# Optimization experiments

Hardware: AMD Instinct MI355X
Metric: run time of the kernel (lower is better)

Reference implementation:

```python
import jax, jax.numpy as jnp
import numpy as np

N = 131072   # total gates/nodes in the batched block-diagonal circuit graph
E = 524288   # directed edges (avg degree 4)
D = 100      # hidden dim
DA = 50      # msg MLP hidden
DC = 30      # classifier hidden
R = 20       # message-passing rounds


def mlp(x, W1, b1, W2, b2):
    return jax.nn.relu(x @ W1 + b1) @ W2 + b2


def gru_step(x, h, Wih, Whh, bih, bhh):
    # single-timestep torch.nn.GRU cell
    gi = x @ Wih.T + bih
    gh = h @ Whh.T + bhh
    ir, iz, inn = jnp.split(gi, 3, axis=-1)
    hr, hz, hn = jnp.split(gh, 3, axis=-1)
    r = jax.nn.sigmoid(ir + hr)
    z = jax.nn.sigmoid(iz + hz)
    nwe = jnp.tanh(inn + r * hn)
    return (1.0 - z) * nwe + z * h


def setup_inputs():
    key = jax.random.key(0)
    ks = jax.random.split(key, 26)
    s = 0.05

    def rn(k, shape):
        return jax.random.normal(k, shape, dtype=jnp.float32) * s

    inp = {
        'features': jax.random.normal(ks[0], (N, 4), dtype=jnp.float32),
        'edge_row': jax.random.randint(ks[1], (E,), 0, N, dtype=jnp.int32),
        'edge_col': jax.random.randint(ks[2], (E,), 0, N, dtype=jnp.int32),
        'init_W': rn(ks[3], (4, D)), 'init_b': jnp.zeros((D,), jnp.float32),
        'fmsg_W1': rn(ks[4], (D, DA)), 'fmsg_b1': jnp.zeros((DA,), jnp.float32),
        'fmsg_W2': rn(ks[5], (DA, D)), 'fmsg_b2': jnp.zeros((D,), jnp.float32),
        'bmsg_W1': rn(ks[6], (D, DA)), 'bmsg_b1': jnp.zeros((DA,), jnp.float32),
        'bmsg_W2': rn(ks[7], (DA, D)), 'bmsg_b2': jnp.zeros((D,), jnp.float32),
        'fgru_Wih': rn(ks[8], (3 * D, D)), 'fgru_Whh': rn(ks[9], (3 * D, D)),
        'fgru_bih': jnp.zeros((3 * D,), jnp.float32), 'fgru_bhh': jnp.zeros((3 * D,), jnp.float32),
        'bgru_Wih': rn(ks[10], (3 * D, D)), 'bgru_Whh': rn(ks[11], (3 * D, D)),
        'bgru_bih': jnp.zeros((3 * D,), jnp.float32), 'bgru_bhh': jnp.zeros((3 * D,), jnp.float32),
        'cls_W1': rn(ks[12], (D, DC)), 'cls_b1': jnp.zeros((DC,), jnp.float32),
        'cls_W2': rn(ks[13], (DC, 1)), 'cls_b2': jnp.zeros((1,), jnp.float32),
    }
    return inp


def reference(features, edge_row, edge_col, init_W, init_b,
              fmsg_W1, fmsg_b1, fmsg_W2, fmsg_b2,
              bmsg_W1, bmsg_b1, bmsg_W2, bmsg_b2,
              fgru_Wih, fgru_Whh, fgru_bih, fgru_bhh,
              bgru_Wih, bgru_Whh, bgru_bih, bgru_bhh,
              cls_W1, cls_b1, cls_W2, cls_b2):
    n = features.shape[0]
    h = features @ init_W + init_b  # [N, D]

    def round_body(h, _):
        # forward pass: adj @ forward_msg(h)
        fm = mlp(h, fmsg_W1, fmsg_b1, fmsg_W2, fmsg_b2)
        f_msg = jax.ops.segment_sum(fm[edge_col], edge_row, num_segments=n)
        h = gru_step(f_msg, h, fgru_Wih, fgru_Whh, fgru_bih, fgru_bhh)
        # backward pass: adj.T @ backward_msg(h)
        bm = mlp(h, bmsg_W1, bmsg_b1, bmsg_W2, bmsg_b2)
        b_msg = jax.ops.segment_sum(bm[edge_row], edge_col, num_segments=n)
        h = gru_step(b_msg, h, bgru_Wih, bgru_Whh, bgru_bih, bgru_bhh)
        return h, None

    h, _ = jax.lax.scan(jax.checkpoint(round_body), h, None, length=R)
    return mlp(h, cls_W1, cls_b1, cls_W2, cls_b2)  # [N, 1]
```

## Files before the change

### kernel.cpp

```cpp
#include <hip/hip_runtime.h>
#include <math.h>

#define Nn 131072
#define Ee 524288

typedef __attribute__((ext_vector_type(8))) short short8;
typedef __attribute__((ext_vector_type(4))) float f32x4;
typedef unsigned short ushort_t;
typedef unsigned int uint32;

__device__ __forceinline__ f32x4 mfma16(short8 a, short8 b, f32x4 c) {
    return __builtin_amdgcn_mfma_f32_16x16x32_bf16(a, b, c, 0, 0, 0);
}

__device__ __forceinline__ uint32 rne_bf16(float x) {
    uint32 u = __float_as_uint(x);
    return (u + 0x7FFFu + ((u >> 16) & 1u)) >> 16;
}

__device__ __forceinline__ void split3(float x, uint32& h, uint32& m, uint32& l) {
    h = rne_bf16(x);
    float hf = __uint_as_float(h << 16);
    float r1 = x - hf;
    m = rne_bf16(r1);
    float mf = __uint_as_float(m << 16);
    float r2 = r1 - mf;
    l = rne_bf16(r2);
}

__global__ void diag_kernel(float* out, float val) {
    int n = blockIdx.x * 256 + threadIdx.x;
    if (n < Nn) out[n] = (n == 0) ? val : 0.f;
}
__global__ void zero_ints(int* p, int n) {
    int i = blockIdx.x * 256 + threadIdx.x;
    if (i < n) p[i] = 0;
}

__global__ void hist_kernel(const int* __restrict__ er, const int* __restrict__ ec,
                            int* __restrict__ cnt_f, int* __restrict__ cnt_b) {
    int e = blockIdx.x * 256 + threadIdx.x;
    atomicAdd(&cnt_f[er[e]], 1);
    atomicAdd(&cnt_b[ec[e]], 1);
}

__global__ __launch_bounds__(1024) void scan_kernel(const int* __restrict__ cnt,
                                                    int* __restrict__ ptr, int n) {
    __shared__ int sums[1024];
    int t = threadIdx.x;
    int chunk = n >> 10;
    int base = t * chunk;
    int s = 0;
    for (int i = 0; i < chunk; i++) s += cnt[base + i];
    sums[t] = s;
    __syncthreads();
    for (int off = 1; off < 1024; off <<= 1) {
        int v = (t >= off) ? sums[t - off] : 0;
        __syncthreads();
        sums[t] += v;
        __syncthreads();
    }
    int run = (t == 0) ? 0 : sums[t - 1];
    for (int i = 0; i < chunk; i++) { ptr[base + i] = run; run += cnt[base + i]; }
    if (t == 1023) ptr[n] = run;
}

__global__ void fill_kernel(const int* __restrict__ er, const int* __restrict__ ec,
                            int* __restrict__ ptr_f, int* __restrict__ ptr_b,
                            int* __restrict__ src_f, int* __restrict__ src_b) {
    int e = blockIdx.x * 256 + threadIdx.x;
    int r = er[e], c = ec[e];
    int p = atomicAdd(&ptr_f[r], 1); src_f[p] = c;
    int q = atomicAdd(&ptr_b[c], 1); src_b[q] = r;
}

__global__ void prep_gru_w(const float* __restrict__ Wih, const float* __restrict__ Whh,
                           const float* __restrict__ bih, const float* __restrict__ bhh,
                           ushort_t* __restrict__ W0, ushort_t* __restrict__ W1,
                           ushort_t* __restrict__ W2, float* __restrict__ bg) {
    int gid = blockIdx.x * 256 + threadIdx.x;
    if (gid >= 448 * 224) return;
    int c = gid / 224, k = gid - c * 224;
    int d = c >> 2, g = c & 3;
    float w = 0.f;
    if (d < 100) {
        if (k < 100) {
            if (g == 0)      w = Wih[d * 100 + k];
            else if (g == 1) w = Wih[(100 + d) * 100 + k];
            else if (g == 2) w = Wih[(200 + d) * 100 + k];
        } else if (k < 200) {
            int kk = k - 100;
            if (g == 0)      w = Whh[d * 100 + kk];
            else if (g == 1) w = Whh[(100 + d) * 100 + kk];
            else if (g == 3) w = Whh[(200 + d) * 100 + kk];
        }
    }
    uint32 h, m, l; split3(w, h, m, l);
    W0[gid] = (ushort_t)h; W1[gid] = (ushort_t)m; W2[gid] = (ushort_t)l;
    if (k == 0) {
        float b = 0.f;
        if (d < 100) {
            if (g == 0)      b = bih[d] + bhh[d];
            else if (g == 1) b = bih[100 + d] + bhh[100 + d];
            else if (g == 2) b = bih[200 + d];
            else             b = bhh[200 + d];
        }
        bg[c] = b;
    }
}

__global__ void prep_msg_w(const float* __restrict__ W1, const float* __restrict__ b1,
                           const float* __restrict__ W2, const float* __restrict__ b2,
                           ushort_t* __restrict__ A0, ushort_t* __restrict__ A1,
                           ushort_t* __restrict__ A2, float* __restrict__ b1p,
                           ushort_t* __restrict__ B0, ushort_t* __restrict__ B1,
                           ushort_t* __restrict__ B2, float* __restrict__ b2p) {
    int gid = blockIdx.x * 256 + threadIdx.x;
    if (gid < 8192) {
        int c = gid >> 7, k = gid & 127;
        float w = (c < 50 && k < 100) ? W1[k * 50 + c] : 0.f;
        uint32 h, m, l; split3(w, h, m, l);
        A0[gid] = (ushort_t)h; A1[gid] = (ushort_t)m; A2[gid] = (ushort_t)l;
        if (k == 0) b1p[c] = (c < 50) ? b1[c] : 0.f;
    } else if (gid < 8192 + 7168) {
        int t = gid - 8192;
        int c = t >> 6, k = t & 63;
        float w = (c < 100 && k < 50) ? W2[k * 100 + c] : 0.f;
        uint32 h, m, l; split3(w, h, m, l);
        B0[t] = (ushort_t)h; B1[t] = (ushort_t)m; B2[t] = (ushort_t)l;
        if (k == 0) b2p[c] = (c < 100) ? b2[c] : 0.f;
    }
}

__global__ void init_h_kernel(const float* __restrict__ feat, const float* __restrict__ W,
                              const float* __restrict__ b, float* __restrict__ Act) {
    int gid = blockIdx.x * 256 + threadIdx.x;
    int n = gid / 100, d = gid - n * 100;
    float acc = b[d];
#pragma unroll
    for (int k = 0; k < 4; k++) acc += feat[n * 4 + k] * W[k * 100 + d];
    Act[(size_t)n * 200 + 100 + d] = acc;
}

__global__ __launch_bounds__(256, 2) void msg_mfma(
    const float* __restrict__ Act,
    const ushort_t* __restrict__ A0, const ushort_t* __restrict__ A1,
    const ushort_t* __restrict__ A2, const float* __restrict__ b1p,
    const ushort_t* __restrict__ B0, const ushort_t* __restrict__ B1,
    const ushort_t* __restrict__ B2, const float* __restrict__ b2p,
    float* __restrict__ fm) {
    __shared__ ushort_t C1[3][64][72];
    const int tid = threadIdx.x;
    const int u = tid >> 6;
    const int lane = tid & 63;
    const int m = lane & 15, q = lane >> 4;
    const int n0 = blockIdx.x * 64;
    const int n = n0 + u * 16 + m;

    f32x4 z = {0.f, 0.f, 0.f, 0.f};
    f32x4 a1[4] = {z, z, z, z};

    for (int kc = 0; kc < 4; kc++) {
        int kb = kc * 32 + q * 8;
        const float* src = Act + (size_t)n * 200 + 100 + kb;
        float4 v0 = *(const float4*)src;
        float4 v1 = *(const float4*)(src + 4);
        float e[8] = {v0.x, v0.y, v0.z, v0.w, v1.x, v1.y, v1.z, v1.w};
        union { short8 s; uint32 u4[4]; } f0, f1, f2;
#pragma unroll
        for (int j = 0; j < 4; j++) {
            uint32 ha, ma, la, hb, mb, lb;
            split3(e[2 * j], ha, ma, la);
            split3(e[2 * j + 1], hb, mb, lb);
            f0.u4[j] = ha | (hb << 16);
            f1.u4[j] = ma | (mb << 16);
            f2.u4[j] = la | (lb << 16);
        }
#pragma unroll
        for (int t = 0; t < 4; t++) {
            int off = (t * 16 + m) * 128 + kc * 32 + q * 8;
            short8 w0 = *(const short8*)(A0 + off);
            short8 w1 = *(const short8*)(A1 + off);
            short8 w2 = *(const short8*)(A2 + off);
            a1[t] = mfma16(w0, f0.s, a1[t]);
            a1[t] = mfma16(w0, f1.s, a1[t]);
            a1[t] = mfma16(w1, f0.s, a1[t]);
            a1[t] = mfma16(w0, f2.s, a1[t]);
            a1[t] = mfma16(w2, f0.s, a1[t]);
            a1[t] = mfma16(w1, f1.s, a1[t]);
        }
    }
#pragma unroll
    for (int t = 0; t < 4; t++) {
        int c0 = t * 16 + 4 * q;
        float4 bb = *(const float4*)&b1p[c0];
        float v0 = fmaxf(a1[t][0] + bb.x, 0.f);
        float v1 = fmaxf(a1[t][1] + bb.y, 0.f);
        float v2 = fmaxf(a1[t][2] + bb.z, 0.f);
        float v3 = fmaxf(a1[t][3] + bb.w, 0.f);
        uint32 h0, m0, l0, h1, m1, l1, h2, m2, l2, h3, m3, l3;
        split3(v0, h0, m0, l0); split3(v1, h1, m1, l1);
        split3(v2, h2, m2, l2); split3(v3, h3, m3, l3);
        int nl = u * 16 + m;
        *(uint2*)&C1[0][nl][c0] = make_uint2(h0 | (h1 << 16), h2 | (h3 << 16));
        *(uint2*)&C1[1][nl][c0] = make_uint2(m0 | (m1 << 16), m2 | (m3 << 16));
        *(uint2*)&C1[2][nl][c0] = make_uint2(l0 | (l1 << 16), l2 | (l3 << 16));
    }
    __syncthreads();

    f32x4 a2[7] = {z, z, z, z, z, z, z};
    for (int kc = 0; kc < 2; kc++) {
        int nl = u * 16 + m;
        short8 c0f = *(const short8*)&C1[0][nl][kc * 32 + q * 8];
        short8 c1f = *(const short8*)&C1[1][nl][kc * 32 + q * 8];
        short8 c2f = *(const short8*)&C1[2][nl][kc * 32 + q * 8];
#pragma unroll
        for (int t = 0; t < 7; t++) {
            int off = (t * 16 + m) * 64 + kc * 32 + q * 8;
            short8 w0 = *(const short8*)(B0 + off);
            short8 w1 = *(const short8*)(B1 + off);
            short8 w2 = *(const short8*)(B2 + off);
            a2[t] = mfma16(w0, c0f, a2[t]);
            a2[t] = mfma16(w0, c1f, a2[t]);
            a2[t] = mfma16(w1, c0f, a2[t]);
            a2[t] = mfma16(w0, c2f, a2[t]);
            a2[t] = mfma16(w2, c0f, a2[t]);
            a2[t] = mfma16(w1, c1f, a2[t]);
        }
    }
#pragma unroll
    for (int t = 0; t < 7; t++) {
        int c0 = t * 16 + 4 * q;
        if (c0 < 100) {
            float4 bb = *(const float4*)&b2p[c0];
            float4 o;
            o.x = a2[t][0] + bb.x; o.y = a2[t][1] + bb.y;
            o.z = a2[t][2] + bb.z; o.w = a2[t][3] + bb.w;
            *(float4*)&fm[(size_t)n * 100 + c0] = o;
        }
    }
}

__global__ void gather4(const float* __restrict__ fm, const int* __restrict__ ptr,
                        const int* __restrict__ idx, float* __restrict__ Act) {
    int gid = blockIdx.x * 256 + threadIdx.x;
    int n = gid / 25, qq = (gid - n * 25) * 4;
    int s = (n == 0) ? 0 : ptr[n - 1];
    int e = ptr[n];
    float4 acc = {0.f, 0.f, 0.f, 0.f};
    for (int i = s; i < e; i++) {
        float4 v = *(const float4*)&fm[(size_t)idx[i] * 100 + qq];
        acc.x += v.x; acc.y += v.y; acc.z += v.z; acc.w += v.w;
    }
    *(float4*)&Act[(size_t)n * 200 + qq] = acc;
}

__global__ __launch_bounds__(256, 2) void gru_mfma(
    float* __restrict__ Act,
    const ushort_t* __restrict__ W0, const ushort_t* __restrict__ W1,
    const ushort_t* __restrict__ W2, const float* __restrict__ bg) {
    __shared__ uint32 Bs[3][64][20];
    const int tid = threadIdx.x;
    const int wave = tid >> 6;
    const int lane = tid & 63;
    const int m = lane & 15, q = lane >> 4;
    const int n0 = blockIdx.x * 64;
    const int sr = tid >> 2;
    const int sk = (tid & 3) * 8;

    f32x4 z = {0.f, 0.f, 0.f, 0.f};
    f32x4 acc[7][4];
#pragma unroll
    for (int t = 0; t < 7; t++)
#pragma unroll
        for (int u = 0; u < 4; u++) acc[t][u] = z;

    for (int kc = 0; kc < 7; kc++) {
        __syncthreads();
        int kb = kc * 32 + sk;
        float e[8];
        if (kb < 200) {
            const float* src = Act + (size_t)(n0 + sr) * 200 + kb;
            float4 v0 = *(const float4*)src;
            float4 v1 = *(const float4*)(src + 4);
            e[0] = v0.x; e[1] = v0.y; e[2] = v0.z; e[3] = v0.w;
            e[4] = v1.x; e[5] = v1.y; e[6] = v1.z; e[7] = v1.w;
        } else {
#pragma unroll
            for (int j = 0; j < 8; j++) e[j] = 0.f;
        }
        uint32 P0[4], P1[4], P2[4];
#pragma unroll
        for (int j = 0; j < 4; j++) {
            uint32 ha, ma, la, hb, mb, lb;
            split3(e[2 * j], ha, ma, la);
            split3(e[2 * j + 1], hb, mb, lb);
            P0[j] = ha | (hb << 16);
            P1[j] = ma | (mb << 16);
            P2[j] = la | (lb << 16);
        }
        *(uint4*)&Bs[0][sr][(tid & 3) * 4] = make_uint4(P0[0], P0[1], P0[2], P0[3]);
        *(uint4*)&Bs[1][sr][(tid & 3) * 4] = make_uint4(P1[0], P1[1], P1[2], P1[3]);
        *(uint4*)&Bs[2][sr][(tid & 3) * 4] = make_uint4(P2[0], P2[1], P2[2], P2[3]);
        __syncthreads();

        short8 bf0[4], bf1[4], bf2[4];
#pragma unroll
        for (int u = 0; u < 4; u++) {
            bf0[u] = *(const short8*)&Bs[0][u * 16 + m][q * 4];
            bf1[u] = *(const short8*)&Bs[1][u * 16 + m][q * 4];
            bf2[u] = *(const short8*)&Bs[2][u * 16 + m][q * 4];
        }
#pragma unroll 2
        for (int t = 0; t < 7; t++) {
            int off = ((wave * 7 + t) * 16 + m) * 224 + kc * 32 + q * 8;
            short8 w0 = *(const short8*)(W0 + off);
            short8 w1 = *(const short8*)(W1 + off);
            short8 w2 = *(const short8*)(W2 + off);
#pragma unroll
            for (int u = 0; u < 4; u++) acc[t][u] = mfma16(w0, bf0[u], acc[t][u]);
#pragma unroll
            for (int u = 0; u < 4; u++) acc[t][u] = mfma16(w0, bf1[u], acc[t][u]);
#pragma unroll
            for (int u = 0; u < 4; u++) acc[t][u] = mfma16(w1, bf0[u], acc[t][u]);
#pragma unroll
            for (int u = 0; u < 4; u++) acc[t][u] = mfma16(w0, bf2[u], acc[t][u]);
#pragma unroll
            for (int u = 0; u < 4; u++) acc[t][u] = mfma16(w2, bf0[u], acc[t][u]);
#pragma unroll
            for (int u = 0; u < 4; u++) acc[t][u] = mfma16(w1, bf1[u], acc[t][u]);
        }
    }

#pragma unroll
    for (int t = 0; t < 7; t++) {
        int c0 = (wave * 7 + t) * 16 + 4 * q;
        int d = c0 >> 2;
        float4 b4 = *(const float4*)&bg[c0];
        if (d < 100) {
#pragma unroll
            for (int u = 0; u < 4; u++) {
                int n = n0 + u * 16 + m;
                float hold = Act[(size_t)n * 200 + 100 + d];
                float rp = acc[t][u][0] + b4.x;
                float zp = acc[t][u][1] + b4.y;
                float np = acc[t][u][2] + b4.z;
                float hp = acc[t][u][3] + b4.w;
                float rr = 1.f / (1.f + __expf(-rp));
                float zz = 1.f / (1.f + __expf(-zp));
                float nw = tanhf(np + rr * hp);
                Act[(size_t)n * 200 + 100 + d] = (1.f - zz) * nw + zz * hold;
            }
        }
    }
}

__global__ __launch_bounds__(256) void classifier(
    const float* __restrict__ Act, const float* __restrict__ W1,
    const float* __restrict__ b1, const float* __restrict__ W2,
    const float* __restrict__ b2, float* __restrict__ out) {
    __shared__ float Wc[3000];
    __shared__ float bc[30];
    __shared__ float w2[30];
    int tid = threadIdx.x;
    for (int i = tid; i < 3000; i += 256) Wc[i] = W1[i];
    if (tid < 30) { bc[tid] = b1[tid]; w2[tid] = W2[tid]; }
    __syncthreads();
    int n = blockIdx.x * 256 + tid;
    float a[30];
#pragma unroll
    for (int j = 0; j < 30; j++) a[j] = bc[j];
    for (int k = 0; k < 100; k++) {
        float hv = Act[(size_t)n * 200 + 100 + k];
#pragma unroll
        for (int j = 0; j < 30; j++) a[j] = fmaf(hv, Wc[k * 30 + j], a[j]);
    }
    float s = b2[0];
#pragma unroll
    for (int j = 0; j < 30; j++) s = fmaf(fmaxf(a[j], 0.f), w2[j], s);
    out[n] = s;
}

extern "C" void kernel_launch(void* const* d_in, const int* in_sizes, int n_in,
                              void* d_out, int out_size, void* d_ws, size_t ws_size,
                              hipStream_t stream) {
    const float* feat     = (const float*)d_in[0];
    const int*   er       = (const int*)d_in[1];
    const int*   ec       = (const int*)d_in[2];
    const float* init_W   = (const float*)d_in[3];
    const float* init_b   = (const float*)d_in[4];
    const float* fmsg_W1  = (const float*)d_in[5];
    const float* fmsg_b1  = (const float*)d_in[6];
    const float* fmsg_W2  = (const float*)d_in[7];
    const float* fmsg_b2  = (const float*)d_in[8];
    const float* bmsg_W1  = (const float*)d_in[9];
    const float* bmsg_b1  = (const float*)d_in[10];
    const float* bmsg_W2  = (const float*)d_in[11];
    const float* bmsg_b2  = (const float*)d_in[12];
    const float* fgru_Wih = (const float*)d_in[13];
    const float* fgru_Whh = (const float*)d_in[14];
    const float* fgru_bih = (const float*)d_in[15];
    const float* fgru_bhh = (const float*)d_in[16];
    const float* bgru_Wih = (const float*)d_in[17];
    const float* bgru_Whh = (const float*)d_in[18];
    const float* bgru_bih = (const float*)d_in[19];
    const float* bgru_bhh = (const float*)d_in[20];
    const float* cls_W1   = (const float*)d_in[21];
    const float* cls_b1   = (const float*)d_in[22];
    const float* cls_W2   = (const float*)d_in[23];
    const float* cls_b2   = (const float*)d_in[24];
    float* out = (float*)d_out;

    float* ws = (float*)d_ws;
    size_t o = 0;
    float* Act = ws + o; o += (size_t)Nn * 200;
    float* fm  = ws + o; o += (size_t)Nn * 100;

    ushort_t* us = (ushort_t*)(ws + o);
    size_t uo = 0;
    ushort_t* fWg0 = us + uo; uo += 448 * 224;
    ushort_t* fWg1 = us + uo; uo += 448 * 224;
    ushort_t* fWg2 = us + uo; uo += 448 * 224;
    ushort_t* bWg0 = us + uo; uo += 448 * 224;
    ushort_t* bWg1 = us + uo; uo += 448 * 224;
    ushort_t* bWg2 = us + uo; uo += 448 * 224;
    ushort_t* fA0 = us + uo; uo += 8192;
    ushort_t* fA1 = us + uo; uo += 8192;
    ushort_t* fA2 = us + uo; uo += 8192;
    ushort_t* bA0 = us + uo; uo += 8192;
    ushort_t* bA1 = us + uo; uo += 8192;
    ushort_t* bA2 = us + uo; uo += 8192;
    ushort_t* fB0 = us + uo; uo += 7168;
    ushort_t* fB1 = us + uo; uo += 7168;
    ushort_t* fB2 = us + uo; uo += 7168;
    ushort_t* bB0 = us + uo; uo += 7168;
    ushort_t* bB1 = us + uo; uo += 7168;
    ushort_t* bB2 = us + uo; uo += 7168;
    o += uo / 2;

    float* bgf  = ws + o; o += 448;
    float* bgb  = ws + o; o += 448;
    float* b1pf = ws + o; o += 64;
    float* b1pb = ws + o; o += 64;
    float* b2pf = ws + o; o += 112;
    float* b2pb = ws + o; o += 112;

    int* iws   = (int*)(ws + o);
    int* ptr_f = iws;
    int* ptr_b = ptr_f + (Nn + 1);
    int* cnt   = ptr_b + (Nn + 1);
    int* cnt_f = cnt;
    int* cnt_b = cnt + Nn;
    int* src_f = cnt + 2 * (size_t)Nn;
    int* src_b = src_f + Ee;

    size_t need = o * sizeof(float) +
                  (size_t)(2 * (Nn + 1) + 2 * Nn + 2 * Ee) * sizeof(int);
    if (ws_size < need) {
        diag_kernel<<<(Nn + 255) / 256, 256, 0, stream>>>(out, (float)ws_size);
        return;
    }

    zero_ints<<<(2 * Nn + 255) / 256, 256, 0, stream>>>(cnt, 2 * Nn);
    hist_kernel<<<Ee / 256, 256, 0, stream>>>(er, ec, cnt_f, cnt_b);
    scan_kernel<<<1, 1024, 0, stream>>>(cnt_f, ptr_f, Nn);
    scan_kernel<<<1, 1024, 0, stream>>>(cnt_b, ptr_b, Nn);
    fill_kernel<<<Ee / 256, 256, 0, stream>>>(er, ec, ptr_f, ptr_b, src_f, src_b);

    prep_gru_w<<<(448 * 224 + 255) / 256, 256, 0, stream>>>(
        fgru_Wih, fgru_Whh, fgru_bih, fgru_bhh, fWg0, fWg1, fWg2, bgf);
    prep_gru_w<<<(448 * 224 + 255) / 256, 256, 0, stream>>>(
        bgru_Wih, bgru_Whh, bgru_bih, bgru_bhh, bWg0, bWg1, bWg2, bgb);
    prep_msg_w<<<(15360 + 255) / 256, 256, 0, stream>>>(
        fmsg_W1, fmsg_b1, fmsg_W2, fmsg_b2, fA0, fA1, fA2, b1pf, fB0, fB1, fB2, b2pf);
    prep_msg_w<<<(15360 + 255) / 256, 256, 0, stream>>>(
        bmsg_W1, bmsg_b1, bmsg_W2, bmsg_b2, bA0, bA1, bA2, b1pb, bB0, bB1, bB2, b2pb);

    init_h_kernel<<<(Nn * 100) / 256, 256, 0, stream>>>(feat, init_W, init_b, Act);

    const int gTile = Nn / 64;
    const int gGath = Nn * 25 / 256;

    for (int rd = 0; rd < 20; rd++) {
        msg_mfma<<<gTile, 256, 0, stream>>>(Act, fA0, fA1, fA2, b1pf, fB0, fB1, fB2, b2pf, fm);
        gather4<<<gGath, 256, 0, stream>>>(fm, ptr_f, src_f, Act);
        gru_mfma<<<gTile, 256, 0, stream>>>(Act, fWg0, fWg1, fWg2, bgf);

        msg_mfma<<<gTile, 256, 0, stream>>>(Act, bA0, bA1, bA2, b1pb, bB0, bB1, bB2, b2pb, fm);
        gather4<<<gGath, 256, 0, stream>>>(fm, ptr_b, src_b, Act);
        gru_mfma<<<gTile, 256, 0, stream>>>(Act, bWg0, bWg1, bWg2, bgb);
    }

    classifier<<<Nn / 256, 256, 0, stream>>>(Act, cls_W1, cls_b1, cls_W2, cls_b2, out);
}
```

Before: 14.61 ms.

## Restructure GRU MFMA kernel with 32-node tiles, double-buffered LDS, and trimmed padding

The GRU kernel now tiles 32 nodes per block instead of 64 and double-buffers the bf16-split activation chunks in shared memory, prefetching the next K chunk while MFMAs run on the current one. Output columns are interleaved across waves and the padded columns beyond 400 are dropped, removing wasted MFMA work on zero rows. The occupancy hint rises to 3 blocks per CU. The trade-off is that each weight fragment is reused across half as many nodes, so global weight traffic per node doubles.

```diff
diff --git a/kernel.cpp b/kernel.cpp
--- a/kernel.cpp
+++ b/kernel.cpp
@@ -79,32 +79,28 @@
                            ushort_t* __restrict__ W0, ushort_t* __restrict__ W1,
                            ushort_t* __restrict__ W2, float* __restrict__ bg) {
     int gid = blockIdx.x * 256 + threadIdx.x;
-    if (gid >= 448 * 224) return;
+    if (gid >= 400 * 224) return;
     int c = gid / 224, k = gid - c * 224;
     int d = c >> 2, g = c & 3;
     float w = 0.f;
-    if (d < 100) {
-        if (k < 100) {
-            if (g == 0)      w = Wih[d * 100 + k];
-            else if (g == 1) w = Wih[(100 + d) * 100 + k];
-            else if (g == 2) w = Wih[(200 + d) * 100 + k];
-        } else if (k < 200) {
-            int kk = k - 100;
-            if (g == 0)      w = Whh[d * 100 + kk];
-            else if (g == 1) w = Whh[(100 + d) * 100 + kk];
-            else if (g == 3) w = Whh[(200 + d) * 100 + kk];
-        }
+    if (k < 100) {
+        if (g == 0)      w = Wih[d * 100 + k];
+        else if (g == 1) w = Wih[(100 + d) * 100 + k];
+        else if (g == 2) w = Wih[(200 + d) * 100 + k];
+    } else if (k < 200) {
+        int kk = k - 100;
+        if (g == 0)      w = Whh[d * 100 + kk];
+        else if (g == 1) w = Whh[(100 + d) * 100 + kk];
+        else if (g == 3) w = Whh[(200 + d) * 100 + kk];
     }
     uint32 h, m, l; split3(w, h, m, l);
     W0[gid] = (ushort_t)h; W1[gid] = (ushort_t)m; W2[gid] = (ushort_t)l;
     if (k == 0) {
-        float b = 0.f;
-        if (d < 100) {
-            if (g == 0)      b = bih[d] + bhh[d];
-            else if (g == 1) b = bih[100 + d] + bhh[100 + d];
-            else if (g == 2) b = bih[200 + d];
-            else             b = bhh[200 + d];
-        }
+        float b;
+        if (g == 0)      b = bih[d] + bhh[d];
+        else if (g == 1) b = bih[100 + d] + bhh[100 + d];
+        else if (g == 2) b = bih[200 + d];
+        else             b = bhh[200 + d];
         bg[c] = b;
     }
 }
@@ -255,101 +251,104 @@
     *(float4*)&Act[(size_t)n * 200 + qq] = acc;
 }
 
-__global__ __launch_bounds__(256, 2) void gru_mfma(
+__global__ __launch_bounds__(256, 3) void gru_mfma(
     float* __restrict__ Act,
     const ushort_t* __restrict__ W0, const ushort_t* __restrict__ W1,
     const ushort_t* __restrict__ W2, const float* __restrict__ bg) {
-    __shared__ uint32 Bs[3][64][20];
+    __shared__ __align__(16) uint32 Bs[2][3][32][20];
     const int tid = threadIdx.x;
     const int wave = tid >> 6;
     const int lane = tid & 63;
     const int m = lane & 15, q = lane >> 4;
-    const int n0 = blockIdx.x * 64;
-    const int sr = tid >> 2;
-    const int sk = (tid & 3) * 8;
+    const int n0 = blockIdx.x * 32;
+    const int sr = tid >> 3;
+    const int sk4 = (tid & 7) * 4;
+    const int cu = (tid & 7) * 2;
 
     f32x4 z = {0.f, 0.f, 0.f, 0.f};
-    f32x4 acc[7][4];
-#pragma unroll
-    for (int t = 0; t < 7; t++)
-#pragma unroll
-        for (int u = 0; u < 4; u++) acc[t][u] = z;
+    f32x4 acc[7][2];
+#pragma unroll
+    for (int t = 0; t < 7; t++) { acc[t][0] = z; acc[t][1] = z; }
+
+    const float* actrow = Act + (size_t)(n0 + sr) * 200;
+
+#define LDCHUNK(kc, dst) do {                                   \
+        int kb = (kc) * 32 + sk4;                               \
+        if (kb < 200) dst = *(const float4*)(actrow + kb);      \
+        else { dst.x = 0.f; dst.y = 0.f; dst.z = 0.f; dst.w = 0.f; } \
+    } while (0)
+
+#define STAGE(b, v) do {                                        \
+        uint32 h0,m0,l0,h1,m1,l1,h2,m2,l2,h3,m3,l3;             \
+        split3((v).x,h0,m0,l0); split3((v).y,h1,m1,l1);         \
+        split3((v).z,h2,m2,l2); split3((v).w,h3,m3,l3);         \
+        *(uint2*)&Bs[b][0][sr][cu] = make_uint2(h0|(h1<<16), h2|(h3<<16)); \
+        *(uint2*)&Bs[b][1][sr][cu] = make_uint2(m0|(m1<<16), m2|(m3<<16)); \
+        *(uint2*)&Bs[b][2][sr][cu] = make_uint2(l0|(l1<<16), l2|(l3<<16)); \
+    } while (0)
+
+    {
+        float4 v0; LDCHUNK(0, v0);
+        STAGE(0, v0);
+    }
+    __syncthreads();
 
     for (int kc = 0; kc < 7; kc++) {
+        float4 nxt;
+        if (kc < 6) LDCHUNK(kc + 1, nxt);
+        const int b = kc & 1;
+        short8 bf0[2], bf1[2], bf2[2];
+#pragma unroll
+        for (int u = 0; u < 2; u++) {
+            bf0[u] = *(const short8*)&Bs[b][0][u * 16 + m][q * 4];
+            bf1[u] = *(const short8*)&Bs[b][1][u * 16 + m][q * 4];
+            bf2[u] = *(const short8*)&Bs[b][2][u * 16 + m][q * 4];
+        }
+#pragma unroll
+        for (int t = 0; t < 7; t++) {
+            if (t < 6 || wave == 0) {
+                const int ct = t * 4 + wave;
+                int off = (ct * 16 + m) * 224 + kc * 32 + q * 8;
+                short8 w0 = *(const short8*)(W0 + off);
+                short8 w1 = *(const short8*)(W1 + off);
+                short8 w2 = *(const short8*)(W2 + off);
+#pragma unroll
+                for (int u = 0; u < 2; u++) {
+                    acc[t][u] = mfma16(w0, bf0[u], acc[t][u]);
+                    acc[t][u] = mfma16(w0, bf1[u], acc[t][u]);
+                    acc[t][u] = mfma16(w1, bf0[u], acc[t][u]);
+                    acc[t][u] = mfma16(w0, bf2[u], acc[t][u]);
+                    acc[t][u] = mfma16(w2, bf0[u], acc[t][u]);
+                    acc[t][u] = mfma16(w1, bf1[u], acc[t][u]);
+                }
+            }
+        }
+        if (kc < 6) STAGE(b ^ 1, nxt);
         __syncthreads();
-        int kb = kc * 32 + sk;
-        float e[8];
-        if (kb < 200) {
-            const float* src = Act + (size_t)(n0 + sr) * 200 + kb;
-            float4 v0 = *(const float4*)src;
-            float4 v1 = *(const float4*)(src + 4);
-            e[0] = v0.x; e[1] = v0.y; e[2] = v0.z; e[3] = v0.w;
-            e[4] = v1.x; e[5] = v1.y; e[6] = v1.z; e[7] = v1.w;
-        } else {
-#pragma unroll
-            for (int j = 0; j < 8; j++) e[j] = 0.f;
-        }
-        uint32 P0[4], P1[4], P2[4];
-#pragma unroll
-        for (int j = 0; j < 4; j++) {
-            uint32 ha, ma, la, hb, mb, lb;
-            split3(e[2 * j], ha, ma, la);
-            split3(e[2 * j + 1], hb, mb, lb);
-            P0[j] = ha | (hb << 16);
-            P1[j] = ma | (mb << 16);
-            P2[j] = la | (lb << 16);
-        }
-        *(uint4*)&Bs[0][sr][(tid & 3) * 4] = make_uint4(P0[0], P0[1], P0[2], P0[3]);
-        *(uint4*)&Bs[1][sr][(tid & 3) * 4] = make_uint4(P1[0], P1[1], P1[2], P1[3]);
-        *(uint4*)&Bs[2][sr][(tid & 3) * 4] = make_uint4(P2[0], P2[1], P2[2], P2[3]);
-        __syncthreads();
-
-        short8 bf0[4], bf1[4], bf2[4];
-#pragma unroll
-        for (int u = 0; u < 4; u++) {
-            bf0[u] = *(const short8*)&Bs[0][u * 16 + m][q * 4];
-            bf1[u] = *(const short8*)&Bs[1][u * 16 + m][q * 4];
-            bf2[u] = *(const short8*)&Bs[2][u * 16 + m][q * 4];
-        }
-#pragma unroll 2
-        for (int t = 0; t < 7; t++) {
-            int off = ((wave * 7 + t) * 16 + m) * 224 + kc * 32 + q * 8;
-            short8 w0 = *(const short8*)(W0 + off);
-            short8 w1 = *(const short8*)(W1 + off);
-            short8 w2 = *(const short8*)(W2 + off);
-#pragma unroll
-            for (int u = 0; u < 4; u++) acc[t][u] = mfma16(w0, bf0[u], acc[t][u]);
-#pragma unroll
-            for (int u = 0; u < 4; u++) acc[t][u] = mfma16(w0, bf1[u], acc[t][u]);
-#pragma unroll
-            for (int u = 0; u < 4; u++) acc[t][u] = mfma16(w1, bf0[u], acc[t][u]);
-#pragma unroll
-            for (int u = 0; u < 4; u++) acc[t][u] = mfma16(w0, bf2[u], acc[t][u]);
-#pragma unroll
-            for (int u = 0; u < 4; u++) acc[t][u] = mfma16(w2, bf0[u], acc[t][u]);
-#pragma unroll
-            for (int u = 0; u < 4; u++) acc[t][u] = mfma16(w1, bf1[u], acc[t][u]);
-        }
-    }
+    }
+#undef LDCHUNK
+#undef STAGE
 
 #pragma unroll
     for (int t = 0; t < 7; t++) {
-        int c0 = (wave * 7 + t) * 16 + 4 * q;
-        int d = c0 >> 2;
-        float4 b4 = *(const float4*)&bg[c0];
-        if (d < 100) {
-#pragma unroll
-            for (int u = 0; u < 4; u++) {
+        if (t < 6 || wave == 0) {
+            const int ct = t * 4 + wave;
+            const int c0 = ct * 16 + 4 * q;
+            const int d = ct * 4 + q;
+            float4 b4 = *(const float4*)&bg[c0];
+#pragma unroll
+            for (int u = 0; u < 2; u++) {
                 int n = n0 + u * 16 + m;
-                float hold = Act[(size_t)n * 200 + 100 + d];
+                float* hp = Act + (size_t)n * 200 + 100 + d;
+                float hold = *hp;
                 float rp = acc[t][u][0] + b4.x;
                 float zp = acc[t][u][1] + b4.y;
                 float np = acc[t][u][2] + b4.z;
-                float hp = acc[t][u][3] + b4.w;
+                float hh = acc[t][u][3] + b4.w;
                 float rr = 1.f / (1.f + __expf(-rp));
                 float zz = 1.f / (1.f + __expf(-zp));
-                float nw = tanhf(np + rr * hp);
-                Act[(size_t)n * 200 + 100 + d] = (1.f - zz) * nw + zz * hold;
+                float nw = tanhf(np + rr * hh);
+                *hp = (1.f - zz) * nw + zz * hold;
             }
         }
     }
@@ -418,12 +417,12 @@
 
     ushort_t* us = (ushort_t*)(ws + o);
     size_t uo = 0;
-    ushort_t* fWg0 = us + uo; uo += 448 * 224;
-    ushort_t* fWg1 = us + uo; uo += 448 * 224;
-    ushort_t* fWg2 = us + uo; uo += 448 * 224;
-    ushort_t* bWg0 = us + uo; uo += 448 * 224;
-    ushort_t* bWg1 = us + uo; uo += 448 * 224;
-    ushort_t* bWg2 = us + uo; uo += 448 * 224;
+    ushort_t* fWg0 = us + uo; uo += 400 * 224;
+    ushort_t* fWg1 = us + uo; uo += 400 * 224;
+    ushort_t* fWg2 = us + uo; uo += 400 * 224;
+    ushort_t* bWg0 = us + uo; uo += 400 * 224;
+    ushort_t* bWg1 = us + uo; uo += 400 * 224;
+    ushort_t* bWg2 = us + uo; uo += 400 * 224;
     ushort_t* fA0 = us + uo; uo += 8192;
     ushort_t* fA1 = us + uo; uo += 8192;
     ushort_t* fA2 = us + uo; uo += 8192;
@@ -438,8 +437,8 @@
     ushort_t* bB2 = us + uo; uo += 7168;
     o += uo / 2;
 
-    float* bgf  = ws + o; o += 448;
-    float* bgb  = ws + o; o += 448;
+    float* bgf  = ws + o; o += 400;
+    float* bgb  = ws + o; o += 400;
     float* b1pf = ws + o; o += 64;
     float* b1pb = ws + o; o += 64;
     float* b2pf = ws + o; o += 112;
@@ -467,9 +466,9 @@
     scan_kernel<<<1, 1024, 0, stream>>>(cnt_b, ptr_b, Nn);
     fill_kernel<<<Ee / 256, 256, 0, stream>>>(er, ec, ptr_f, ptr_b, src_f, src_b);
 
-    prep_gru_w<<<(448 * 224 + 255) / 256, 256, 0, stream>>>(
+    prep_gru_w<<<(400 * 224 + 255) / 256, 256, 0, stream>>>(
         fgru_Wih, fgru_Whh, fgru_bih, fgru_bhh, fWg0, fWg1, fWg2, bgf);
-    prep_gru_w<<<(448 * 224 + 255) / 256, 256, 0, stream>>>(
+    prep_gru_w<<<(400 * 224 + 255) / 256, 256, 0, stream>>>(
         bgru_Wih, bgru_Whh, bgru_bih, bgru_bhh, bWg0, bWg1, bWg2, bgb);
     prep_msg_w<<<(15360 + 255) / 256, 256, 0, stream>>>(
         fmsg_W1, fmsg_b1, fmsg_W2, fmsg_b2, fA0, fA1, fA2, b1pf, fB0, fB1, fB2, b2pf);
@@ -479,16 +478,17 @@
     init_h_kernel<<<(Nn * 100) / 256, 256, 0, stream>>>(feat, init_W, init_b, Act);
 
     const int gTile = Nn / 64;
+    const int gGru  = Nn / 32;
     const int gGath = Nn * 25 / 256;
 
     for (int rd = 0; rd < 20; rd++) {
         msg_mfma<<<gTile, 256, 0, stream>>>(Act, fA0, fA1, fA2, b1pf, fB0, fB1, fB2, b2pf, fm);
         gather4<<<gGath, 256, 0, stream>>>(fm, ptr_f, src_f, Act);
-        gru_mfma<<<gTile, 256, 0, stream>>>(Act, fWg0, fWg1, fWg2, bgf);
+        gru_mfma<<<gGru, 256, 0, stream>>>(Act, fWg0, fWg1, fWg2, bgf);
 
         msg_mfma<<<gTile, 256, 0, stream>>>(Act, bA0, bA1, bA2, b1pb, bB0, bB1, bB2, b2pb, fm);
         gather4<<<gGath, 256, 0, stream>>>(fm, ptr_b, src_b, Act);
-        gru_mfma<<<gTile, 256, 0, stream>>>(Act, bWg0, bWg1, bWg2, bgb);
+        gru_mfma<<<gGru, 256, 0, stream>>>(Act, bWg0, bWg1, bWg2, bgb);
     }
 
     classifier<<<Nn / 256, 256, 0, stream>>>(Act, cls_W1, cls_b1, cls_W2, cls_b2, out);
```

Result: faster. 14.28 ms (-2.3%).

## Load GRU activations straight into registers and drop LDS staging

Applied to the files above, without the earlier changes.

The GRU MFMA kernel no longer stages the bf16 three-way-split activations through shared memory with two barriers per K chunk. Instead each wave loads its 64 node rows from global memory and splits them into MFMA fragments itself. Output tiles are now interleaved across waves, and the MFMA passes are regrouped so each weight split is loaded once per chunk and reused across passes. The cost is that all four waves repeat the same global loads and split arithmetic, and register pressure goes up. A single barrier is kept before the in-place hidden-state write so no wave overwrites state another wave is still reading.

```diff
diff --git a/kernel.cpp b/kernel.cpp
--- a/kernel.cpp
+++ b/kernel.cpp
@@ -259,97 +259,101 @@
     float* __restrict__ Act,
     const ushort_t* __restrict__ W0, const ushort_t* __restrict__ W1,
     const ushort_t* __restrict__ W2, const float* __restrict__ bg) {
-    __shared__ uint32 Bs[3][64][20];
     const int tid = threadIdx.x;
     const int wave = tid >> 6;
     const int lane = tid & 63;
     const int m = lane & 15, q = lane >> 4;
     const int n0 = blockIdx.x * 64;
-    const int sr = tid >> 2;
-    const int sk = (tid & 3) * 8;
 
     f32x4 z = {0.f, 0.f, 0.f, 0.f};
     f32x4 acc[7][4];
 #pragma unroll
     for (int t = 0; t < 7; t++)
 #pragma unroll
-        for (int u = 0; u < 4; u++) acc[t][u] = z;
+        for (int rf = 0; rf < 4; rf++) acc[t][rf] = z;
+
+    int woff[7];
+#pragma unroll
+    for (int t = 0; t < 7; t++)
+        woff[t] = ((t * 4 + wave) * 16 + m) * 224 + q * 8;
+
+    const float* abase = Act + (size_t)(n0 + m) * 200 + q * 8;
+
+#define GPASS(Wreg, Fr)                                          \
+    _Pragma("unroll")                                            \
+    for (int t = 0; t < 7; t++) {                                \
+        _Pragma("unroll")                                        \
+        for (int rf = 0; rf < 4; rf++)                           \
+            acc[t][rf] = mfma16(Wreg[t], Fr[rf], acc[t][rf]);    \
+    }
 
     for (int kc = 0; kc < 7; kc++) {
-        __syncthreads();
-        int kb = kc * 32 + sk;
-        float e[8];
-        if (kb < 200) {
-            const float* src = Act + (size_t)(n0 + sr) * 200 + kb;
-            float4 v0 = *(const float4*)src;
-            float4 v1 = *(const float4*)(src + 4);
-            e[0] = v0.x; e[1] = v0.y; e[2] = v0.z; e[3] = v0.w;
-            e[4] = v1.x; e[5] = v1.y; e[6] = v1.z; e[7] = v1.w;
-        } else {
-#pragma unroll
-            for (int j = 0; j < 8; j++) e[j] = 0.f;
-        }
-        uint32 P0[4], P1[4], P2[4];
-#pragma unroll
-        for (int j = 0; j < 4; j++) {
-            uint32 ha, ma, la, hb, mb, lb;
-            split3(e[2 * j], ha, ma, la);
-            split3(e[2 * j + 1], hb, mb, lb);
-            P0[j] = ha | (hb << 16);
-            P1[j] = ma | (mb << 16);
-            P2[j] = la | (lb << 16);
-        }
-        *(uint4*)&Bs[0][sr][(tid & 3) * 4] = make_uint4(P0[0], P0[1], P0[2], P0[3]);
-        *(uint4*)&Bs[1][sr][(tid & 3) * 4] = make_uint4(P1[0], P1[1], P1[2], P1[3]);
-        *(uint4*)&Bs[2][sr][(tid & 3) * 4] = make_uint4(P2[0], P2[1], P2[2], P2[3]);
-        __syncthreads();
-
-        short8 bf0[4], bf1[4], bf2[4];
-#pragma unroll
-        for (int u = 0; u < 4; u++) {
-            bf0[u] = *(const short8*)&Bs[0][u * 16 + m][q * 4];
-            bf1[u] = *(const short8*)&Bs[1][u * 16 + m][q * 4];
-            bf2[u] = *(const short8*)&Bs[2][u * 16 + m][q * 4];
-        }
-#pragma unroll 2
-        for (int t = 0; t < 7; t++) {
-            int off = ((wave * 7 + t) * 16 + m) * 224 + kc * 32 + q * 8;
-            short8 w0 = *(const short8*)(W0 + off);
-            short8 w1 = *(const short8*)(W1 + off);
-            short8 w2 = *(const short8*)(W2 + off);
-#pragma unroll
-            for (int u = 0; u < 4; u++) acc[t][u] = mfma16(w0, bf0[u], acc[t][u]);
-#pragma unroll
-            for (int u = 0; u < 4; u++) acc[t][u] = mfma16(w0, bf1[u], acc[t][u]);
-#pragma unroll
-            for (int u = 0; u < 4; u++) acc[t][u] = mfma16(w1, bf0[u], acc[t][u]);
-#pragma unroll
-            for (int u = 0; u < 4; u++) acc[t][u] = mfma16(w0, bf2[u], acc[t][u]);
-#pragma unroll
-            for (int u = 0; u < 4; u++) acc[t][u] = mfma16(w2, bf0[u], acc[t][u]);
-#pragma unroll
-            for (int u = 0; u < 4; u++) acc[t][u] = mfma16(w1, bf1[u], acc[t][u]);
-        }
-    }
+        const int kb = kc * 32 + q * 8;
+        const int ko = kc * 32;
+        short8 f0[4], f1[4], f2[4];
+#pragma unroll
+        for (int rf = 0; rf < 4; rf++) {
+            float e[8];
+            if (kb < 200) {
+                const float* src = abase + (size_t)rf * 16 * 200 + ko;
+                float4 v0 = *(const float4*)src;
+                float4 v1 = *(const float4*)(src + 4);
+                e[0] = v0.x; e[1] = v0.y; e[2] = v0.z; e[3] = v0.w;
+                e[4] = v1.x; e[5] = v1.y; e[6] = v1.z; e[7] = v1.w;
+            } else {
+#pragma unroll
+                for (int j = 0; j < 8; j++) e[j] = 0.f;
+            }
+            union { short8 s; uint32 u4[4]; } p0, p1, p2;
+#pragma unroll
+            for (int j = 0; j < 4; j++) {
+                uint32 ha, ma, la, hb, mb, lb;
+                split3(e[2 * j], ha, ma, la);
+                split3(e[2 * j + 1], hb, mb, lb);
+                p0.u4[j] = ha | (hb << 16);
+                p1.u4[j] = ma | (mb << 16);
+                p2.u4[j] = la | (lb << 16);
+            }
+            f0[rf] = p0.s; f1[rf] = p1.s; f2[rf] = p2.s;
+        }
+
+        short8 w[7];
+#pragma unroll
+        for (int t = 0; t < 7; t++) w[t] = *(const short8*)(W0 + woff[t] + ko);
+        GPASS(w, f0);
+        GPASS(w, f1);
+        GPASS(w, f2);
+#pragma unroll
+        for (int t = 0; t < 7; t++) w[t] = *(const short8*)(W1 + woff[t] + ko);
+        GPASS(w, f0);
+        GPASS(w, f1);
+#pragma unroll
+        for (int t = 0; t < 7; t++) w[t] = *(const short8*)(W2 + woff[t] + ko);
+        GPASS(w, f0);
+    }
+#undef GPASS
+
+    __syncthreads();
 
 #pragma unroll
     for (int t = 0; t < 7; t++) {
-        int c0 = (wave * 7 + t) * 16 + 4 * q;
-        int d = c0 >> 2;
-        float4 b4 = *(const float4*)&bg[c0];
+        const int ct = t * 4 + wave;
+        const int d = ct * 4 + q;
         if (d < 100) {
-#pragma unroll
-            for (int u = 0; u < 4; u++) {
-                int n = n0 + u * 16 + m;
-                float hold = Act[(size_t)n * 200 + 100 + d];
-                float rp = acc[t][u][0] + b4.x;
-                float zp = acc[t][u][1] + b4.y;
-                float np = acc[t][u][2] + b4.z;
-                float hp = acc[t][u][3] + b4.w;
+            float4 b4 = *(const float4*)&bg[ct * 16 + 4 * q];
+#pragma unroll
+            for (int rf = 0; rf < 4; rf++) {
+                int n = n0 + rf * 16 + m;
+                float* hp = Act + (size_t)n * 200 + 100 + d;
+                float hold = *hp;
+                float rp = acc[t][rf][0] + b4.x;
+                float zp = acc[t][rf][1] + b4.y;
+                float np = acc[t][rf][2] + b4.z;
+                float hh = acc[t][rf][3] + b4.w;
                 float rr = 1.f / (1.f + __expf(-rp));
                 float zz = 1.f / (1.f + __expf(-zp));
-                float nw = tanhf(np + rr * hp);
-                Act[(size_t)n * 200 + 100 + d] = (1.f - zz) * nw + zz * hold;
+                float nw = tanhf(np + rr * hh);
+                *hp = (1.f - zz) * nw + zz * hold;
             }
         }
     }
@@ -479,16 +483,17 @@
     init_h_kernel<<<(Nn * 100) / 256, 256, 0, stream>>>(feat, init_W, init_b, Act);
 
     const int gTile = Nn / 64;
+    const int gGru  = Nn / 64;
     const int gGath = Nn * 25 / 256;
 
     for (int rd = 0; rd < 20; rd++) {
         msg_mfma<<<gTile, 256, 0, stream>>>(Act, fA0, fA1, fA2, b1pf, fB0, fB1, fB2, b2pf, fm);
         gather4<<<gGath, 256, 0, stream>>>(fm, ptr_f, src_f, Act);
-        gru_mfma<<<gTile, 256, 0, stream>>>(Act, fWg0, fWg1, fWg2, bgf);
+        gru_mfma<<<gGru, 256, 0, stream>>>(Act, fWg0, fWg1, fWg2, bgf);
 
         msg_mfma<<<gTile, 256, 0, stream>>>(Act, bA0, bA1, bA2, b1pb, bB0, bB1, bB2, b2pb, fm);
         gather4<<<gGath, 256, 0, stream>>>(fm, ptr_b, src_b, Act);
-        gru_mfma<<<gTile, 256, 0, stream>>>(Act, bWg0, bWg1, bWg2, bgb);
+        gru_mfma<<<gGru, 256, 0, stream>>>(Act, bWg0, bWg1, bWg2, bgb);
     }
 
     classifier<<<Nn / 256, 256, 0, stream>>>(Act, cls_W1, cls_b1, cls_W2, cls_b2, out);
```

New measurement: 13.68 ms. -6.4%, faster.
